# Optimization experiments

Hardware: AMD Instinct MI355X
Metric: run time of the kernel (lower is better)

Reference implementation:

```python
import jax, jax.numpy as jnp
import numpy as np


def setup_inputs() -> dict:
    key = jax.random.key(0)
    k1, k2, k3 = jax.random.split(key, 3)
    N, T_OBS, T_FUT, D = 100000, 16, 14, 66
    observed_pose = jax.random.normal(k1, (1, T_OBS, D), dtype=jnp.float32)
    train_pose = jax.random.normal(k2, (N, T_OBS, D), dtype=jnp.float32)
    train_future_pose = jax.random.normal(k3, (N, T_FUT, D), dtype=jnp.float32)
    return {
        "observed_pose": observed_pose,
        "train_pose": train_pose,
        "train_future_pose": train_future_pose,
    }


def reference(observed_pose, train_pose, train_future_pose):
    # query velocity: [1, (T_obs-1)*D]
    in_vel = (observed_pose[..., 1:, :] - observed_pose[..., :-1, :]).reshape(1, -1)
    # database velocities: [N, (T_obs-1)*D]
    N = train_pose.shape[0]
    tr_vel = (train_pose[..., 1:, :] - train_pose[..., :-1, :]).reshape(N, -1)
    # MSELoss(reduction='none').sum(1) == squared L2 distance per sample
    diff = tr_vel - in_vel  # broadcast query over N
    dis = jnp.sum(diff * diff, axis=1)  # [N]
    ind = jnp.argmin(dis)
    pred_pose = train_future_pose[ind][None]  # [1, T_fut, D]
    return pred_pose
```

## Files before the change

kernel.cpp:

```cpp
#include <hip/hip_runtime.h>
#include <cstdint>

#define ROW   1056
#define ROW2  528
#define VEL2  495
#define FUT   924

__global__ void nn_init(unsigned long long* best) {
    if (threadIdx.x == 0 && blockIdx.x == 0)
        *best = 0xFFFFFFFFFFFFFFFFull;
}

__global__ __launch_bounds__(256, 4) void nn_dist(const float* __restrict__ obs,
                                                  const float* __restrict__ train,
                                                  int N,
                                                  unsigned long long* best) {
    const int lane = threadIdx.x & 63;
    const int wave = threadIdx.x >> 6;
    const int wpb  = blockDim.x >> 6;
    const long long gwave   = (long long)blockIdx.x * wpb + wave;
    const long long wstride = (long long)gridDim.x * wpb;

    const float2* __restrict__ obs2 = (const float2*)obs;
    const float2* __restrict__ tr2  = (const float2*)train;

    const bool t7 = (lane < (VEL2 - 448));
    float qx[8], qy[8];
    #pragma unroll
    for (int k = 0; k < 7; ++k) {
        int j = lane + 64 * k;
        float2 a = obs2[j], b = obs2[j + 33];
        qx[k] = b.x - a.x;  qy[k] = b.y - a.y;
    }
    if (t7) {
        int j = lane + 448;
        float2 a = obs2[j], b = obs2[j + 33];
        qx[7] = b.x - a.x;  qy[7] = b.y - a.y;
    } else { qx[7] = 0.f; qy[7] = 0.f; }

    unsigned long long bestKey = 0xFFFFFFFFFFFFFFFFull;

    for (long long n = 2 * gwave; n < N; n += 2 * wstride) {
        const bool have1 = (n + 1 < N);
        const float2* __restrict__ r0 = tr2 + n * ROW2;
        const float2* __restrict__ r1 = have1 ? (r0 + ROW2) : r0;

        float s0 = 0.f, s1 = 0.f;
        #pragma unroll
        for (int k = 0; k < 7; ++k) {
            int j = lane + 64 * k;
            float2 a0 = r0[j], b0 = r0[j + 33];
            float2 a1 = r1[j], b1 = r1[j + 33];
            float dx0 = b0.x - a0.x - qx[k], dy0 = b0.y - a0.y - qy[k];
            float dx1 = b1.x - a1.x - qx[k], dy1 = b1.y - a1.y - qy[k];
            s0 += dx0 * dx0 + dy0 * dy0;
            s1 += dx1 * dx1 + dy1 * dy1;
        }
        if (t7) {
            int j = lane + 448;
            float2 a0 = r0[j], b0 = r0[j + 33];
            float2 a1 = r1[j], b1 = r1[j + 33];
            float dx0 = b0.x - a0.x - qx[7], dy0 = b0.y - a0.y - qy[7];
            float dx1 = b1.x - a1.x - qx[7], dy1 = b1.y - a1.y - qy[7];
            s0 += dx0 * dx0 + dy0 * dy0;
            s1 += dx1 * dx1 + dy1 * dy1;
        }

        #pragma unroll
        for (int off = 32; off > 0; off >>= 1) {
            s0 += __shfl_xor(s0, off, 64);
            s1 += __shfl_xor(s1, off, 64);
        }

        unsigned long long k0 =
            ((unsigned long long)__float_as_uint(s0) << 32) | (unsigned)n;
        if (k0 < bestKey) bestKey = k0;
        if (have1) {
            unsigned long long k1 =
                ((unsigned long long)__float_as_uint(s1) << 32) | (unsigned)(n + 1);
            if (k1 < bestKey) bestKey = k1;
        }
    }

    __shared__ unsigned long long wbest[4];
    if (lane == 0) wbest[wave] = bestKey;
    __syncthreads();
    if (threadIdx.x == 0) {
        unsigned long long k0 = wbest[0];
        for (int w = 1; w < wpb; ++w)
            k0 = (wbest[w] < k0) ? wbest[w] : k0;
        atomicMin(best, k0);
    }
}

__global__ void nn_gather(const unsigned long long* best,
                          const float* __restrict__ fut,
                          float* __restrict__ out) {
    const int idx = (int)(unsigned)(*best & 0xFFFFFFFFull);
    const float4* __restrict__ src = (const float4*)(fut + (long long)idx * FUT);
    float4* __restrict__ dst = (float4*)out;
    for (int i = threadIdx.x; i < FUT / 4; i += blockDim.x)
        dst[i] = src[i];
}

extern "C" void kernel_launch(void* const* d_in, const int* in_sizes, int n_in,
                              void* d_out, int out_size, void* d_ws, size_t ws_size,
                              hipStream_t stream) {
    const float* obs   = (const float*)d_in[0];
    const float* train = (const float*)d_in[1];
    const float* fut   = (const float*)d_in[2];
    float* out = (float*)d_out;
    const int N = in_sizes[1] / ROW;

    unsigned long long* best = (unsigned long long*)d_ws;

    nn_init<<<1, 64, 0, stream>>>(best);
    nn_dist<<<2048, 256, 0, stream>>>(obs, train, N, best);
    nn_gather<<<1, 256, 0, stream>>>(best, fut, out);
}
```

Baseline: 684.0 us.

## Load each training row once and form shifted values via cross-lane shuffles

Each row is now read once into registers as nine coalesced float2 chunks, and the time-shifted operand (offset 33 float2s) is taken from neighbouring lanes with shuffles instead of a second overlapping global load. This halves the load instructions per row, which were largely redundant cache hits. Separately, the init kernel and the global atomicMin are replaced by per-block partial results that a single final kernel reduces before gathering the output, saving one launch. The cost is extra shuffle and select instructions plus higher register use.

```diff
diff --git a/kernel.cpp b/kernel.cpp
--- a/kernel.cpp
+++ b/kernel.cpp
@@ -5,26 +5,24 @@
 #define ROW2  528
 #define VEL2  495
 #define FUT   924
-
-__global__ void nn_init(unsigned long long* best) {
-    if (threadIdx.x == 0 && blockIdx.x == 0)
-        *best = 0xFFFFFFFFFFFFFFFFull;
-}
+#define GRID  2048
 
 __global__ __launch_bounds__(256, 4) void nn_dist(const float* __restrict__ obs,
                                                   const float* __restrict__ train,
                                                   int N,
-                                                  unsigned long long* best) {
+                                                  unsigned long long* __restrict__ blockBest) {
     const int lane = threadIdx.x & 63;
     const int wave = threadIdx.x >> 6;
-    const int wpb  = blockDim.x >> 6;
-    const long long gwave   = (long long)blockIdx.x * wpb + wave;
-    const long long wstride = (long long)gridDim.x * wpb;
+    const long long gwave   = (long long)blockIdx.x * 4 + wave;
+    const long long wstride = (long long)gridDim.x * 4;
 
     const float2* __restrict__ obs2 = (const float2*)obs;
     const float2* __restrict__ tr2  = (const float2*)train;
 
-    const bool t7 = (lane < (VEL2 - 448));
+    const bool t7      = (lane < (VEL2 - 448));
+    const int  bsrc    = (lane + 33) & 63;
+    const bool lowHalf = (lane < 31);
+
     float qx[8], qy[8];
     #pragma unroll
     for (int k = 0; k < 7; ++k) {
@@ -45,25 +43,32 @@
         const float2* __restrict__ r0 = tr2 + n * ROW2;
         const float2* __restrict__ r1 = have1 ? (r0 + ROW2) : r0;
 
+        float2 A0[9], A1[9];
+        #pragma unroll
+        for (int k = 0; k < 8; ++k) {
+            A0[k] = r0[lane + 64 * k];
+            A1[k] = r1[lane + 64 * k];
+        }
+        A0[8] = r0[512 + (lane & 15)];
+        A1[8] = r1[512 + (lane & 15)];
+
         float s0 = 0.f, s1 = 0.f;
+        float sx0 = __shfl(A0[0].x, bsrc, 64), sy0 = __shfl(A0[0].y, bsrc, 64);
+        float sx1 = __shfl(A1[0].x, bsrc, 64), sy1 = __shfl(A1[0].y, bsrc, 64);
         #pragma unroll
-        for (int k = 0; k < 7; ++k) {
-            int j = lane + 64 * k;
-            float2 a0 = r0[j], b0 = r0[j + 33];
-            float2 a1 = r1[j], b1 = r1[j + 33];
-            float dx0 = b0.x - a0.x - qx[k], dy0 = b0.y - a0.y - qy[k];
-            float dx1 = b1.x - a1.x - qx[k], dy1 = b1.y - a1.y - qy[k];
-            s0 += dx0 * dx0 + dy0 * dy0;
-            s1 += dx1 * dx1 + dy1 * dy1;
-        }
-        if (t7) {
-            int j = lane + 448;
-            float2 a0 = r0[j], b0 = r0[j + 33];
-            float2 a1 = r1[j], b1 = r1[j + 33];
-            float dx0 = b0.x - a0.x - qx[7], dy0 = b0.y - a0.y - qy[7];
-            float dx1 = b1.x - a1.x - qx[7], dy1 = b1.y - a1.y - qy[7];
-            s0 += dx0 * dx0 + dy0 * dy0;
-            s1 += dx1 * dx1 + dy1 * dy1;
+        for (int k = 0; k < 8; ++k) {
+            float nx0 = __shfl(A0[k + 1].x, bsrc, 64), ny0 = __shfl(A0[k + 1].y, bsrc, 64);
+            float nx1 = __shfl(A1[k + 1].x, bsrc, 64), ny1 = __shfl(A1[k + 1].y, bsrc, 64);
+            float bx0 = lowHalf ? sx0 : nx0, by0 = lowHalf ? sy0 : ny0;
+            float bx1 = lowHalf ? sx1 : nx1, by1 = lowHalf ? sy1 : ny1;
+            float dx0 = bx0 - A0[k].x - qx[k], dy0 = by0 - A0[k].y - qy[k];
+            float dx1 = bx1 - A1[k].x - qx[k], dy1 = by1 - A1[k].y - qy[k];
+            bool valid = (k < 7) || t7;
+            if (valid) {
+                s0 += dx0 * dx0 + dy0 * dy0;
+                s1 += dx1 * dx1 + dy1 * dy1;
+            }
+            sx0 = nx0; sy0 = ny0; sx1 = nx1; sy1 = ny1;
         }
 
         #pragma unroll
@@ -87,16 +92,39 @@
     __syncthreads();
     if (threadIdx.x == 0) {
         unsigned long long k0 = wbest[0];
-        for (int w = 1; w < wpb; ++w)
+        #pragma unroll
+        for (int w = 1; w < 4; ++w)
             k0 = (wbest[w] < k0) ? wbest[w] : k0;
-        atomicMin(best, k0);
+        blockBest[blockIdx.x] = k0;
     }
 }
 
-__global__ void nn_gather(const unsigned long long* best,
-                          const float* __restrict__ fut,
-                          float* __restrict__ out) {
-    const int idx = (int)(unsigned)(*best & 0xFFFFFFFFull);
+__global__ __launch_bounds__(256) void nn_final(const unsigned long long* __restrict__ blockBest,
+                                                int nb,
+                                                const float* __restrict__ fut,
+                                                float* __restrict__ out) {
+    const int lane = threadIdx.x & 63;
+    const int wave = threadIdx.x >> 6;
+
+    unsigned long long k = 0xFFFFFFFFFFFFFFFFull;
+    for (int i = threadIdx.x; i < nb; i += 256) {
+        unsigned long long v = blockBest[i];
+        if (v < k) k = v;
+    }
+    #pragma unroll
+    for (int off = 32; off > 0; off >>= 1) {
+        unsigned long long o = __shfl_xor(k, off, 64);
+        if (o < k) k = o;
+    }
+    __shared__ unsigned long long ws[4];
+    if (lane == 0) ws[wave] = k;
+    __syncthreads();
+    unsigned long long fk = ws[0];
+    #pragma unroll
+    for (int w = 1; w < 4; ++w)
+        fk = (ws[w] < fk) ? ws[w] : fk;
+
+    const int idx = (int)(unsigned)(fk & 0xFFFFFFFFull);
     const float4* __restrict__ src = (const float4*)(fut + (long long)idx * FUT);
     float4* __restrict__ dst = (float4*)out;
     for (int i = threadIdx.x; i < FUT / 4; i += blockDim.x)
@@ -112,9 +140,8 @@
     float* out = (float*)d_out;
     const int N = in_sizes[1] / ROW;
 
-    unsigned long long* best = (unsigned long long*)d_ws;
+    unsigned long long* blockBest = (unsigned long long*)d_ws;
 
-    nn_init<<<1, 64, 0, stream>>>(best);
-    nn_dist<<<2048, 256, 0, stream>>>(obs, train, N, best);
-    nn_gather<<<1, 256, 0, stream>>>(best, fut, out);
+    nn_dist<<<GRID, 256, 0, stream>>>(obs, train, N, blockBest);
+    nn_final<<<1, 256, 0, stream>>>(blockBest, GRID, fut, out);
 }
```

Result: no change. 678.9 us (-0.7%).
